# Optimization experiments

Measured on AMD Instinct MI355X. Metric: run time of the kernel, lower is better.

## Reference

```python
import jax, jax.numpy as jnp
import numpy as np

EPS = 1e-6

def elu_feature_map(x):
    return jax.nn.elu(x) + 1.0

def setup_inputs() -> dict:
    key = jax.random.key(0)
    kq, kk, kv = jax.random.split(key, 3)
    N, L, S, H, D = 8, 8192, 8192, 8, 32
    return {
        "queries": jax.random.normal(kq, (N, L, H, D), dtype=jnp.float32),
        "keys": jax.random.normal(kk, (N, S, H, D), dtype=jnp.float32),
        "values": jax.random.normal(kv, (N, S, H, D), dtype=jnp.float32),
    }

def reference(queries, keys, values):
    # Linear (kernelized) attention, default path of MixAttention.forward
    Q = elu_feature_map(queries)            # [N,L,H,D]
    K = elu_feature_map(keys)               # [N,S,H,D]
    v_length = values.shape[1]
    vals = values / v_length                # [N,S,H,D]
    KV = jnp.einsum('nshd,nshv->nhdv', K, vals)          # [N,H,D,D]
    Z = 1.0 / (jnp.einsum('nlhd,nhd->nlh', Q, K.sum(axis=1)) + EPS)  # [N,L,H]
    out = jnp.einsum('nlhd,nhdv,nlh->nlhv', Q, KV, Z) * v_length     # [N,L,H,D]
    return out
```

## Files before the change

kernel.cpp:

```cpp
#include <hip/hip_runtime.h>


constexpr int N_ = 8, L_ = 8192, S_ = 8192, H_ = 8, D_ = 32;
constexpr int NH = N_ * H_;
constexpr int SPLIT = 32;
constexpr int CS = S_ / SPLIT;
constexpr int PART_STRIDE = D_ * D_ + D_;
constexpr int LCH = 256;
constexpr float EPS_ = 1e-6f;
constexpr int HD = H_ * D_;

__device__ __forceinline__ float fmap(float x) {
    return x > 0.0f ? x + 1.0f : __expf(x);
}

__global__ __launch_bounds__(256, 4) void lin_attn_phase1(
        const float* __restrict__ Kg, const float* __restrict__ Vg,
        float* __restrict__ part) {
    const int blk = blockIdx.x;
    const int nh = blk / SPLIT;
    const int sc = blk % SPLIT;
    const int n = nh / H_, h = nh % H_;
    const int t = threadIdx.x;
    const int w = t >> 6;
    const int j = t & 63;
    const int half = j >> 5;
    const int jj = j & 31;
    const int d0 = (jj & 7) << 2;
    const int v0 = (jj >> 3) << 3;

    __shared__ __align__(16) float red[4][1024];
    __shared__ __align__(16) float ksum_red[4][32];

    float acc[4][8];
    #pragma unroll
    for (int a = 0; a < 4; ++a)
        #pragma unroll
        for (int b = 0; b < 8; ++b) acc[a][b] = 0.0f;
    float kp[4] = {0.f, 0.f, 0.f, 0.f};

    const size_t base = (size_t)n * S_ * H_ * D_ + (size_t)h * D_;
    const int s0 = sc * CS;
    const float* kr = Kg + base + (size_t)(s0 + (w << 1) + half) * HD + d0;
    const float* vr = Vg + base + (size_t)(s0 + (w << 1) + half) * HD + v0;
    constexpr int STRIDE = 8 * HD;

#define BEAT(kq, va, vb) do {                                                  \
        float kd[4];                                                           \
        kd[0] = fmap((kq).x); kd[1] = fmap((kq).y);                            \
        kd[2] = fmap((kq).z); kd[3] = fmap((kq).w);                            \
        kp[0] += kd[0]; kp[1] += kd[1]; kp[2] += kd[2]; kp[3] += kd[3];        \
        const float vs[8] = {(va).x, (va).y, (va).z, (va).w,                   \
                             (vb).x, (vb).y, (vb).z, (vb).w};                  \
        _Pragma("unroll")                                                      \
        for (int a = 0; a < 4; ++a)                                            \
            _Pragma("unroll")                                                  \
            for (int bb = 0; bb < 8; ++bb)                                     \
                acc[a][bb] += kd[a] * vs[bb];                                  \
    } while (0)

    float4 kqA = *reinterpret_cast<const float4*>(kr);
    float4 vaA = *reinterpret_cast<const float4*>(vr);
    float4 vbA = *reinterpret_cast<const float4*>(vr + 4);
    float4 kqB = *reinterpret_cast<const float4*>(kr + STRIDE);
    float4 vaB = *reinterpret_cast<const float4*>(vr + STRIDE);
    float4 vbB = *reinterpret_cast<const float4*>(vr + STRIDE + 4);
    kr += 2 * STRIDE; vr += 2 * STRIDE;

    #pragma unroll 1
    for (int b = 0; b < (CS / 8 - 2) / 2; ++b) {
        float4 kqn = *reinterpret_cast<const float4*>(kr);
        float4 van = *reinterpret_cast<const float4*>(vr);
        float4 vbn = *reinterpret_cast<const float4*>(vr + 4);
        BEAT(kqA, vaA, vbA);
        kqA = kqn; vaA = van; vbA = vbn;
        kqn = *reinterpret_cast<const float4*>(kr + STRIDE);
        van = *reinterpret_cast<const float4*>(vr + STRIDE);
        vbn = *reinterpret_cast<const float4*>(vr + STRIDE + 4);
        BEAT(kqB, vaB, vbB);
        kqB = kqn; vaB = van; vbB = vbn;
        kr += 2 * STRIDE; vr += 2 * STRIDE;
    }
    BEAT(kqA, vaA, vbA);
    BEAT(kqB, vaB, vbB);
#undef BEAT

    #pragma unroll
    for (int a = 0; a < 4; ++a)
        #pragma unroll
        for (int bb = 0; bb < 8; ++bb)
            acc[a][bb] += __shfl_xor(acc[a][bb], 32);
    #pragma unroll
    for (int a = 0; a < 4; ++a) kp[a] += __shfl_xor(kp[a], 32);

    if (j < 32) {
        #pragma unroll
        for (int a = 0; a < 4; ++a) {
            *reinterpret_cast<float4*>(&red[w][(d0 + a) * D_ + v0]) =
                make_float4(acc[a][0], acc[a][1], acc[a][2], acc[a][3]);
            *reinterpret_cast<float4*>(&red[w][(d0 + a) * D_ + v0 + 4]) =
                make_float4(acc[a][4], acc[a][5], acc[a][6], acc[a][7]);
        }
        if (j < 8)
            *reinterpret_cast<float4*>(&ksum_red[w][j << 2]) =
                make_float4(kp[0], kp[1], kp[2], kp[3]);
    }
    __syncthreads();

    float* P = part + ((size_t)sc * NH + nh) * PART_STRIDE;
    const int i4 = t << 2;
    float4 s = make_float4(0.f, 0.f, 0.f, 0.f);
    #pragma unroll
    for (int w2 = 0; w2 < 4; ++w2) {
        const float4 rr = *reinterpret_cast<const float4*>(&red[w2][i4]);
        s.x += rr.x; s.y += rr.y; s.z += rr.z; s.w += rr.w;
    }
    *reinterpret_cast<float4*>(&P[i4]) = s;
    if (t < D_) {
        float ks = 0.f;
        #pragma unroll
        for (int w2 = 0; w2 < 4; ++w2) ks += ksum_red[w2][t];
        P[D_ * D_ + t] = ks;
    }
}

__global__ __launch_bounds__(256) void lin_attn_reduce(
        const float* __restrict__ part, float* __restrict__ red) {
    const int i = blockIdx.x * 256 + threadIdx.x;
    if (i >= NH * PART_STRIDE) return;
    float s = 0.0f;
    #pragma unroll
    for (int sc = 0; sc < SPLIT; ++sc)
        s += part[(size_t)sc * (NH * PART_STRIDE) + i];
    red[i] = s;
}

__global__ __launch_bounds__(256) void lin_attn_phase2(
        const float* __restrict__ Qg, const float* __restrict__ red,
        float* __restrict__ outg) {
    constexpr int QTS = 32;
    constexpr int NLC = L_ / LCH;
    const int nh  = blockIdx.x / NLC;
    const int lcb = blockIdx.x % NLC;
    const int n = nh / H_, h = nh % H_;
    const int t = threadIdx.x;
    const int v  = t & 31;
    const int rb = t >> 5;
    const int r  = t >> 3;
    const int c  = (t & 7) << 2;

    __shared__ __align__(16) float Qt[QTS][D_];
    __shared__ float zinv_sh[QTS];

    float kv[D_];
    const float* W = red + (size_t)nh * PART_STRIDE;
    #pragma unroll
    for (int d = 0; d < D_; ++d) kv[d] = W[d * D_ + v];
    const float4 ksq = *reinterpret_cast<const float4*>(W + D_ * D_ + c);

    const size_t base = (size_t)n * L_ * H_ * D_ + (size_t)h * D_;
    const int l0 = lcb * LCH;
    for (int step = 0; step < LCH; step += QTS) {
        const float4 q4 = *reinterpret_cast<const float4*>(
            Qg + base + (size_t)(l0 + step + r) * (H_ * D_) + c);
        __syncthreads();
        float4 qf;
        qf.x = fmap(q4.x); qf.y = fmap(q4.y);
        qf.z = fmap(q4.z); qf.w = fmap(q4.w);
        *reinterpret_cast<float4*>(&Qt[r][c]) = qf;
        float zp = qf.x * ksq.x + qf.y * ksq.y + qf.z * ksq.z + qf.w * ksq.w;
        zp += __shfl_xor(zp, 1);
        zp += __shfl_xor(zp, 2);
        zp += __shfl_xor(zp, 4);
        if ((t & 7) == 0) zinv_sh[r] = 1.0f / (zp + EPS_);
        __syncthreads();
        #pragma unroll
        for (int rr = 0; rr < 4; ++rr) {
            const int row = (rr << 3) + rb;
            float acc = 0.0f;
            #pragma unroll
            for (int d2 = 0; d2 < 16; ++d2) {
                const float2 q = *reinterpret_cast<const float2*>(&Qt[row][d2 << 1]);
                acc += q.x * kv[(d2 << 1)] + q.y * kv[(d2 << 1) + 1];
            }
            outg[base + (size_t)(l0 + step + row) * (H_ * D_) + v] =
                acc * zinv_sh[row];
        }
    }
}

extern "C" void kernel_launch(void* const* d_in, const int* in_sizes, int n_in,
                              void* d_out, int out_size, void* d_ws, size_t ws_size,
                              hipStream_t stream) {
    const float* Q = (const float*)d_in[0];
    const float* K = (const float*)d_in[1];
    const float* V = (const float*)d_in[2];
    float* out  = (float*)d_out;
    float* part = (float*)d_ws;
    float* red  = part + (size_t)SPLIT * NH * PART_STRIDE;

    lin_attn_phase1<<<NH * SPLIT, 256, 0, stream>>>(K, V, part);
    lin_attn_reduce<<<(NH * PART_STRIDE + 255) / 256, 256, 0, stream>>>(part, red);
    lin_attn_phase2<<<NH * (L_ / LCH), 256, 0, stream>>>(Q, red, out);
}
```

Measured before the change: 85.85 us.

## Remap phase1 so each block covers all heads of a row chunk, drop LDS reduce

Phase1 now launches 512-thread blocks where each of the 8 wavefronts handles one head, and each block covers all heads of a contiguous sequence chunk, so every block reads full contiguous K/V rows. Each wave writes its own partial directly to the workspace, which removes the shared-memory cross-wave reduction and its barrier. The split factor becomes a template parameter and uses 64 when the workspace is large enough, which doubles the partial-sum traffic that the reduce kernel has to read.

```diff
diff --git a/kernel.cpp b/kernel.cpp
--- a/kernel.cpp
+++ b/kernel.cpp
@@ -3,8 +3,6 @@
 
 constexpr int N_ = 8, L_ = 8192, S_ = 8192, H_ = 8, D_ = 32;
 constexpr int NH = N_ * H_;
-constexpr int SPLIT = 32;
-constexpr int CS = S_ / SPLIT;
 constexpr int PART_STRIDE = D_ * D_ + D_;
 constexpr int LCH = 256;
 constexpr float EPS_ = 1e-6f;
@@ -14,13 +12,14 @@
     return x > 0.0f ? x + 1.0f : __expf(x);
 }
 
-__global__ __launch_bounds__(256, 4) void lin_attn_phase1(
+template<int SPLIT>
+__global__ __launch_bounds__(512, 4) void lin_attn_phase1(
         const float* __restrict__ Kg, const float* __restrict__ Vg,
         float* __restrict__ part) {
+    constexpr int CS = S_ / SPLIT;
     const int blk = blockIdx.x;
-    const int nh = blk / SPLIT;
+    const int n  = blk / SPLIT;
     const int sc = blk % SPLIT;
-    const int n = nh / H_, h = nh % H_;
     const int t = threadIdx.x;
     const int w = t >> 6;
     const int j = t & 63;
@@ -29,9 +28,6 @@
     const int d0 = (jj & 7) << 2;
     const int v0 = (jj >> 3) << 3;
 
-    __shared__ __align__(16) float red[4][1024];
-    __shared__ __align__(16) float ksum_red[4][32];
-
     float acc[4][8];
     #pragma unroll
     for (int a = 0; a < 4; ++a)
@@ -39,11 +35,11 @@
         for (int b = 0; b < 8; ++b) acc[a][b] = 0.0f;
     float kp[4] = {0.f, 0.f, 0.f, 0.f};
 
-    const size_t base = (size_t)n * S_ * H_ * D_ + (size_t)h * D_;
-    const int s0 = sc * CS;
-    const float* kr = Kg + base + (size_t)(s0 + (w << 1) + half) * HD + d0;
-    const float* vr = Vg + base + (size_t)(s0 + (w << 1) + half) * HD + v0;
-    constexpr int STRIDE = 8 * HD;
+    const size_t base = (size_t)n * S_ * HD
+                      + (size_t)(sc * CS + half) * HD + w * D_;
+    const float* kr = Kg + base + d0;
+    const float* vr = Vg + base + v0;
+    constexpr int STRIDE = 2 * HD;
 
 #define BEAT(kq, va, vb) do {                                                  \
         float kd[4];                                                           \
@@ -68,7 +64,7 @@
     kr += 2 * STRIDE; vr += 2 * STRIDE;
 
     #pragma unroll 1
-    for (int b = 0; b < (CS / 8 - 2) / 2; ++b) {
+    for (int b = 0; b < (CS / 2 - 2) / 2; ++b) {
         float4 kqn = *reinterpret_cast<const float4*>(kr);
         float4 van = *reinterpret_cast<const float4*>(vr);
         float4 vbn = *reinterpret_cast<const float4*>(vr + 4);
@@ -94,42 +90,27 @@
     for (int a = 0; a < 4; ++a) kp[a] += __shfl_xor(kp[a], 32);
 
     if (j < 32) {
+        float* P = part + ((size_t)sc * NH + n * H_ + w) * PART_STRIDE;
         #pragma unroll
         for (int a = 0; a < 4; ++a) {
-            *reinterpret_cast<float4*>(&red[w][(d0 + a) * D_ + v0]) =
+            *reinterpret_cast<float4*>(&P[(d0 + a) * D_ + v0]) =
                 make_float4(acc[a][0], acc[a][1], acc[a][2], acc[a][3]);
-            *reinterpret_cast<float4*>(&red[w][(d0 + a) * D_ + v0 + 4]) =
+            *reinterpret_cast<float4*>(&P[(d0 + a) * D_ + v0 + 4]) =
                 make_float4(acc[a][4], acc[a][5], acc[a][6], acc[a][7]);
         }
         if (j < 8)
-            *reinterpret_cast<float4*>(&ksum_red[w][j << 2]) =
+            *reinterpret_cast<float4*>(&P[D_ * D_ + (j << 2)]) =
                 make_float4(kp[0], kp[1], kp[2], kp[3]);
-    }
-    __syncthreads();
-
-    float* P = part + ((size_t)sc * NH + nh) * PART_STRIDE;
-    const int i4 = t << 2;
-    float4 s = make_float4(0.f, 0.f, 0.f, 0.f);
-    #pragma unroll
-    for (int w2 = 0; w2 < 4; ++w2) {
-        const float4 rr = *reinterpret_cast<const float4*>(&red[w2][i4]);
-        s.x += rr.x; s.y += rr.y; s.z += rr.z; s.w += rr.w;
-    }
-    *reinterpret_cast<float4*>(&P[i4]) = s;
-    if (t < D_) {
-        float ks = 0.f;
-        #pragma unroll
-        for (int w2 = 0; w2 < 4; ++w2) ks += ksum_red[w2][t];
-        P[D_ * D_ + t] = ks;
     }
 }
 
+template<int SPLIT>
 __global__ __launch_bounds__(256) void lin_attn_reduce(
         const float* __restrict__ part, float* __restrict__ red) {
     const int i = blockIdx.x * 256 + threadIdx.x;
     if (i >= NH * PART_STRIDE) return;
     float s = 0.0f;
-    #pragma unroll
+    #pragma unroll 8
     for (int sc = 0; sc < SPLIT; ++sc)
         s += part[(size_t)sc * (NH * PART_STRIDE) + i];
     red[i] = s;
@@ -197,9 +178,19 @@
     const float* V = (const float*)d_in[2];
     float* out  = (float*)d_out;
     float* part = (float*)d_ws;
-    float* red  = part + (size_t)SPLIT * NH * PART_STRIDE;
 
-    lin_attn_phase1<<<NH * SPLIT, 256, 0, stream>>>(K, V, part);
-    lin_attn_reduce<<<(NH * PART_STRIDE + 255) / 256, 256, 0, stream>>>(part, red);
-    lin_attn_phase2<<<NH * (L_ / LCH), 256, 0, stream>>>(Q, red, out);
+    const size_t need64 = ((size_t)64 + 1) * NH * PART_STRIDE * sizeof(float);
+    if (ws_size >= need64) {
+        constexpr int SP = 64;
+        float* red = part + (size_t)SP * NH * PART_STRIDE;
+        lin_attn_phase1<SP><<<N_ * SP, 512, 0, stream>>>(K, V, part);
+        lin_attn_reduce<SP><<<(NH * PART_STRIDE + 255) / 256, 256, 0, stream>>>(part, red);
+        lin_attn_phase2<<<NH * (L_ / LCH), 256, 0, stream>>>(Q, red, out);
+    } else {
+        constexpr int SP = 32;
+        float* red = part + (size_t)SP * NH * PART_STRIDE;
+        lin_attn_phase1<SP><<<N_ * SP, 512, 0, stream>>>(K, V, part);
+        lin_attn_reduce<SP><<<(NH * PART_STRIDE + 255) / 256, 256, 0, stream>>>(part, red);
+        lin_attn_phase2<<<NH * (L_ / LCH), 256, 0, stream>>>(Q, red, out);
+    }
 }
```

After: 88.48 us. 3.1% more time.
